# Optimization experiments

Measured on AMD Instinct MI355X. Metric: run time of the kernel, lower is better.

## Reference

```python
import jax, jax.numpy as jnp
import numpy as np

B, S, D, H = 1, 2048, 2048, 16
HD = D // H  # head_dim = 128
EPS = 1e-6


def setup_inputs() -> dict:
    key = jax.random.key(0)
    ks = jax.random.split(key, 12)
    sc = 0.02
    x = jax.random.normal(ks[0], (B, S, D), jnp.float32)
    wq = jax.random.normal(ks[1], (D, D), jnp.float32) * sc
    bq = jnp.zeros((D,), jnp.float32)
    wk = jax.random.normal(ks[2], (D, D), jnp.float32) * sc
    bk = jnp.zeros((D,), jnp.float32)
    wv = jax.random.normal(ks[3], (D, D), jnp.float32) * sc
    bv = jnp.zeros((D,), jnp.float32)
    wo = jax.random.normal(ks[4], (D, D), jnp.float32) * sc
    bo = jnp.zeros((D,), jnp.float32)
    gq = jnp.ones((D,), jnp.float32)  # RMSNorm weight for q
    gk = jnp.ones((D,), jnp.float32)  # RMSNorm weight for k
    # Rotary frequency table: complex freqs = cos + i*sin, shape [S, 1, HD//2]
    pos = jnp.arange(S, dtype=jnp.float32)
    inv = 1.0 / (10000.0 ** (jnp.arange(0, HD, 2, dtype=jnp.float32) / HD))  # [HD//2]
    theta = pos[:, None] * inv[None, :]  # [S, HD//2]
    freqs_cos = jnp.cos(theta)[:, None, :]  # [S, 1, HD//2]
    freqs_sin = jnp.sin(theta)[:, None, :]
    return {"x": x, "wq": wq, "bq": bq, "wk": wk, "bk": bk, "wv": wv, "bv": bv,
            "wo": wo, "bo": bo, "gq": gq, "gk": gk,
            "freqs_cos": freqs_cos, "freqs_sin": freqs_sin}


def _rmsnorm(x, g):
    # RMSNorm over full model dim (applied BEFORE head split, as in source)
    return x * jax.lax.rsqrt(jnp.mean(x * x, axis=-1, keepdims=True) + EPS) * g


def _rope(x, cos, sin):
    # x: [B,S,D] -> (B,S,H,HD//2,2) complex pairs; complex mult by (cos + i sin)
    b, s, d = x.shape
    xr = x.reshape(b, s, H, HD // 2, 2)
    a, bb = xr[..., 0], xr[..., 1]
    # cos/sin [S,1,HD//2] broadcast against [B,S,H,HD//2]
    ra = a * cos - bb * sin
    rb = a * sin + bb * cos
    return jnp.stack([ra, rb], axis=-1).reshape(b, s, d)


def reference(x, wq, bq, wk, bk, wv, bv, wo, bo, gq, gk, freqs_cos, freqs_sin):
    b, s, d = x.shape
    q = _rope(_rmsnorm(x @ wq.T + bq, gq), freqs_cos, freqs_sin)
    k = _rope(_rmsnorm(x @ wk.T + bk, gk), freqs_cos, freqs_sin)
    v = x @ wv.T + bv
    qh = q.reshape(b, s, H, HD).transpose(0, 2, 1, 3)  # [B,H,S,HD]
    kh = k.reshape(b, s, H, HD).transpose(0, 2, 1, 3)
    vh = v.reshape(b, s, H, HD).transpose(0, 2, 1, 3)
    scores = jnp.einsum('bhqd,bhkd->bhqk', qh, kh) / np.sqrt(HD).astype(np.float32)
    attn = jax.nn.softmax(scores, axis=-1)
    out = jnp.einsum('bhqk,bhkd->bhqd', attn, vh)
    out = out.transpose(0, 2, 1, 3).reshape(b, s, d)
    return out @ wo.T + bo
```

## Files before the change

kernel.cpp:

```cpp
#include <hip/hip_runtime.h>
#include <math.h>

typedef unsigned short u16;
typedef unsigned int u32;
typedef __bf16 bf16x8 __attribute__((ext_vector_type(8)));
typedef float f32x4 __attribute__((ext_vector_type(4)));
typedef float f32x16 __attribute__((ext_vector_type(16)));

__device__ __forceinline__ u16 f2bf(float f) {
  unsigned u = __float_as_uint(f);
  u += 0x7fff + ((u >> 16) & 1);
  return (u16)(u >> 16);
}

__device__ __forceinline__ u32 cvtpk(float lo, float hi) {
  u32 r;
  asm("v_cvt_pk_bf16_f32 %0, %1, %2" : "=v"(r) : "v"(lo), "v"(hi));
  return r;
}

__device__ __forceinline__ void pswap(u32& x, u32& y) {
  asm volatile("v_permlane32_swap_b32 %0, %1" : "+v"(x), "+v"(y));
}

__device__ __forceinline__ void gload_lds16(const void* g, void* l) {
  __builtin_amdgcn_global_load_lds(
      (const __attribute__((address_space(1))) unsigned int*)g,
      (__attribute__((address_space(3))) unsigned int*)l, 16, 0, 0);
}

__global__ __launch_bounds__(256) void k_cvt5(const float* __restrict__ s0,
                                              const float* __restrict__ s1,
                                              const float* __restrict__ s2,
                                              const float* __restrict__ s3,
                                              const float* __restrict__ s4,
                                              u16* __restrict__ dx,
                                              u16* __restrict__ dqkv,
                                              u16* __restrict__ dwo) {
  const int y = blockIdx.y;
  const float* s = (y == 0) ? s0 : (y == 1) ? s1 : (y == 2) ? s2
                   : (y == 3) ? s3 : s4;
  u16* d = (y == 0) ? dx : (y == 4) ? dwo : dqkv + (size_t)(y - 1) * 4194304;
  int i = (blockIdx.x * 256 + threadIdx.x) * 4;
  float4 v = *(const float4*)(s + i);
  ushort4 o;
  o.x = f2bf(v.x); o.y = f2bf(v.y); o.z = f2bf(v.z); o.w = f2bf(v.w);
  *(ushort4*)(d + i) = o;
}

__global__ __launch_bounds__(512, 4) void k_gemm_big(const u16* __restrict__ A,
                                                     const u16* __restrict__ B,
                                                     float* __restrict__ C,
                                                     int M, int N, int K) {
  __shared__ __align__(16) char lds[2][40960];
  const int tid = threadIdx.x;
  const int wid = tid >> 6, lane = tid & 63;
  const int lr = lane & 15, lg = lane >> 4;
  const int wm = (wid >> 2) * 64, wn = (wid & 3) * 48;
  const int nbx = N / 192, nby = M >> 7;
  const int colsPerXcd = nbx >> 3;
  const int xcd = blockIdx.x & 7, idx = blockIdx.x >> 3;
  const int bx = xcd * colsPerXcd + idx / nby;
  const int by = idx % nby;
  const int bm = by * 128, bn = bx * 192;
  const int srow = tid >> 3;
  const int schunk = (tid & 7) ^ (srow & 7);
  const size_t rsK = (size_t)K * 2;
  const char* gA = (const char*)A + (size_t)(bm + srow) * rsK + schunk * 16;
  const char* gB = (const char*)B + (size_t)(bn + srow) * rsK + schunk * 16;
  char* dA = (char*)lds + wid * 1024;
  char* dB = (char*)lds + 16384 + wid * 1024;

#define STAGE(cur, k0)                                                         \
  {                                                                            \
    _Pragma("unroll") for (int i = 0; i < 2; ++i)                              \
        gload_lds16(gA + (size_t)(i * 64) * rsK + (size_t)(k0) * 2,            \
                    dA + (cur) * 40960 + i * 8192);                            \
    _Pragma("unroll") for (int i = 0; i < 3; ++i)                              \
        gload_lds16(gB + (size_t)(i * 64) * rsK + (size_t)(k0) * 2,            \
                    dB + (cur) * 40960 + i * 8192);                            \
  }

  f32x4 acc[4][3] = {};
  STAGE(0, 0);
  STAGE(1, 64);
  asm volatile("s_waitcnt vmcnt(5)" ::: "memory");
  __builtin_amdgcn_s_barrier();
  const int NT = K >> 6;
  int cur = 0;
  const int rsw = (lr & 7);
  for (int t = 0; t < NT; ++t) {
    const char* La = (const char*)lds + cur * 40960;
    const char* Lb = La + 16384;
    bf16x8 af[4][2], bfr[3][2];
#pragma unroll
    for (int mi = 0; mi < 4; ++mi)
#pragma unroll
      for (int kk = 0; kk < 2; ++kk)
        af[mi][kk] = *(const bf16x8*)(La + (wm + mi * 16 + lr) * 128 +
                                      (((kk * 4 + lg) ^ rsw) * 16));
#pragma unroll
    for (int ni = 0; ni < 3; ++ni)
#pragma unroll
      for (int kk = 0; kk < 2; ++kk)
        bfr[ni][kk] = *(const bf16x8*)(Lb + (wn + ni * 16 + lr) * 128 +
                                       (((kk * 4 + lg) ^ rsw) * 16));
    asm volatile("s_waitcnt lgkmcnt(0)" ::: "memory");
    __builtin_amdgcn_s_barrier();
    if (t + 2 < NT) STAGE(cur, (t + 2) << 6);
    __builtin_amdgcn_s_setprio(1);
#pragma unroll
    for (int kk = 0; kk < 2; ++kk)
#pragma unroll
      for (int mi = 0; mi < 4; ++mi)
#pragma unroll
        for (int ni = 0; ni < 3; ++ni)
          acc[mi][ni] = __builtin_amdgcn_mfma_f32_16x16x32_bf16(
              af[mi][kk], bfr[ni][kk], acc[mi][ni], 0, 0, 0);
    __builtin_amdgcn_s_setprio(0);
    if (t + 2 < NT)
      asm volatile("s_waitcnt vmcnt(5)" ::: "memory");
    else
      asm volatile("s_waitcnt vmcnt(0)" ::: "memory");
    __builtin_amdgcn_s_barrier();
    cur ^= 1;
  }
#undef STAGE
#pragma unroll
  for (int mi = 0; mi < 4; ++mi)
#pragma unroll
    for (int ni = 0; ni < 3; ++ni)
#pragma unroll
      for (int j = 0; j < 4; ++j)
        C[(size_t)(bm + wm + mi * 16 + lg * 4 + j) * N + bn + wn + ni * 16 + lr] =
            acc[mi][ni][j];
}

__global__ __launch_bounds__(256, 2) void k_gemm_pipe(const u16* __restrict__ A,
                                                      const u16* __restrict__ B,
                                                      const float* __restrict__ bias,
                                                      float* __restrict__ C,
                                                      int M, int N, int K) {
  __shared__ __align__(16) char lds[2][24576];
  const int tid = threadIdx.x;
  const int wid = tid >> 6, lane = tid & 63;
  const int lr = lane & 15, lg = lane >> 4;
  const int wm = (wid >> 1) * 64, wn = (wid & 1) * 32;
  const int nbx = N >> 6, nby = M >> 7;
  const int colsPerXcd = nbx >> 3;
  const int xcd = blockIdx.x & 7, idx = blockIdx.x >> 3;
  const int bx = xcd * colsPerXcd + idx / nby;
  const int by = idx % nby;
  const int bm = by * 128, bn = bx * 64;
  const int srow = tid >> 3;
  const int schunk = (tid & 7) ^ (srow & 7);
  const size_t rsK = (size_t)K * 2;
  const char* gA = (const char*)A + (size_t)(bm + srow) * rsK + schunk * 16;
  const char* gB = (const char*)B + (size_t)(bn + srow) * rsK + schunk * 16;
  char* dA = (char*)lds + wid * 1024;
  char* dB = (char*)lds + 16384 + wid * 1024;

#define STAGE(cur, k0)                                                         \
  {                                                                            \
    _Pragma("unroll") for (int i = 0; i < 4; ++i)                              \
        gload_lds16(gA + (size_t)(i * 32) * rsK + (size_t)(k0) * 2,            \
                    dA + (cur) * 24576 + i * 4096);                            \
    _Pragma("unroll") for (int i = 0; i < 2; ++i)                              \
        gload_lds16(gB + (size_t)(i * 32) * rsK + (size_t)(k0) * 2,            \
                    dB + (cur) * 24576 + i * 4096);                            \
  }

  f32x4 acc[4][2] = {};
  STAGE(0, 0);
  STAGE(1, 64);
  asm volatile("s_waitcnt vmcnt(6)" ::: "memory");
  __builtin_amdgcn_s_barrier();
  const int NT = K >> 6;
  int cur = 0;
  const int rsw = (lr & 7);
  for (int t = 0; t < NT; ++t) {
    const char* La = (const char*)lds + cur * 24576;
    const char* Lb = La + 16384;
    bf16x8 af[4][2], bfr[2][2];
#pragma unroll
    for (int mi = 0; mi < 4; ++mi)
#pragma unroll
      for (int kk = 0; kk < 2; ++kk)
        af[mi][kk] = *(const bf16x8*)(La + (wm + mi * 16 + lr) * 128 +
                                      (((kk * 4 + lg) ^ rsw) * 16));
#pragma unroll
    for (int ni = 0; ni < 2; ++ni)
#pragma unroll
      for (int kk = 0; kk < 2; ++kk)
        bfr[ni][kk] = *(const bf16x8*)(Lb + (wn + ni * 16 + lr) * 128 +
                                       (((kk * 4 + lg) ^ rsw) * 16));
    asm volatile("s_waitcnt lgkmcnt(0)" ::: "memory");
    __builtin_amdgcn_s_barrier();
    if (t + 2 < NT) STAGE(cur, (t + 2) << 6);
    __builtin_amdgcn_s_setprio(1);
#pragma unroll
    for (int kk = 0; kk < 2; ++kk)
#pragma unroll
      for (int mi = 0; mi < 4; ++mi)
#pragma unroll
        for (int ni = 0; ni < 2; ++ni)
          acc[mi][ni] = __builtin_amdgcn_mfma_f32_16x16x32_bf16(
              af[mi][kk], bfr[ni][kk], acc[mi][ni], 0, 0, 0);
    __builtin_amdgcn_s_setprio(0);
    if (t + 2 < NT)
      asm volatile("s_waitcnt vmcnt(6)" ::: "memory");
    else
      asm volatile("s_waitcnt vmcnt(0)" ::: "memory");
    __builtin_amdgcn_s_barrier();
    cur ^= 1;
  }
#undef STAGE
#pragma unroll
  for (int mi = 0; mi < 4; ++mi)
#pragma unroll
    for (int ni = 0; ni < 2; ++ni) {
      int col = bn + wn + ni * 16 + lr;
      float bb = bias[col];
#pragma unroll
      for (int j = 0; j < 4; ++j)
        C[(size_t)(bm + wm + mi * 16 + lg * 4 + j) * N + col] =
            acc[mi][ni][j] + bb;
    }
}

__global__ __launch_bounds__(256) void k_rmsnorm_rope(
    const float* __restrict__ qkv, const float* __restrict__ bq,
    const float* __restrict__ bk, const float* __restrict__ gq,
    const float* __restrict__ gk, const float* __restrict__ fcos,
    const float* __restrict__ fsin, u16* __restrict__ qb, u16* __restrict__ kb) {
  const int s = blockIdx.x, which = blockIdx.y;
  const int t = threadIdx.x;
  const float* src = qkv + (size_t)s * 6144 + which * 2048;
  const float* bias = which ? bk : bq;
  const float* g = which ? gk : gq;
  u16* dst = (which ? kb : qb) + (size_t)s * 2048;
  const int c0 = t * 8;
  float4 a0 = *(const float4*)(src + c0);
  float4 a1 = *(const float4*)(src + c0 + 4);
  float4 b0 = *(const float4*)(bias + c0);
  float4 b1 = *(const float4*)(bias + c0 + 4);
  float v[8];
  v[0] = a0.x + b0.x; v[1] = a0.y + b0.y; v[2] = a0.z + b0.z; v[3] = a0.w + b0.w;
  v[4] = a1.x + b1.x; v[5] = a1.y + b1.y; v[6] = a1.z + b1.z; v[7] = a1.w + b1.w;
  float ss = 0.f;
#pragma unroll
  for (int j = 0; j < 8; ++j) ss += v[j] * v[j];
#pragma unroll
  for (int m = 1; m < 64; m <<= 1) ss += __shfl_xor(ss, m);
  __shared__ float red[4];
  if ((t & 63) == 0) red[t >> 6] = ss;
  __syncthreads();
  float r = rsqrtf((red[0] + red[1] + red[2] + red[3]) * (1.0f / 2048.0f) + 1e-6f);
  if (!which) r *= 0.08838834764831843f * 1.4426950408889634f;
  float4 g0 = *(const float4*)(g + c0);
  float4 g1 = *(const float4*)(g + c0 + 4);
  float gg[8] = {g0.x, g0.y, g0.z, g0.w, g1.x, g1.y, g1.z, g1.w};
  const int p0 = (c0 & 127) >> 1;
  u16 o[8];
#pragma unroll
  for (int j = 0; j < 4; ++j) {
    float a = v[2 * j] * r * gg[2 * j];
    float b = v[2 * j + 1] * r * gg[2 * j + 1];
    float co = fcos[s * 64 + p0 + j], si = fsin[s * 64 + p0 + j];
    o[2 * j]     = f2bf(a * co - b * si);
    o[2 * j + 1] = f2bf(a * si + b * co);
  }
  ushort4 q0; q0.x = o[0]; q0.y = o[1]; q0.z = o[2]; q0.w = o[3];
  ushort4 q1; q1.x = o[4]; q1.y = o[5]; q1.z = o[6]; q1.w = o[7];
  *(ushort4*)(dst + c0) = q0;
  *(ushort4*)(dst + c0 + 4) = q1;
}

__global__ __launch_bounds__(256) void k_transpose_v(const float* __restrict__ qkv,
                                                     const float* __restrict__ bv,
                                                     u16* __restrict__ vT) {
  __shared__ float tile[64][65];
  const int s0 = blockIdx.x * 64, d0 = blockIdx.y * 64;
  const int t = threadIdx.x;
  const int tc = (t & 15) * 4, tr = t >> 4;
  float4 bb = *(const float4*)(bv + d0 + tc);
#pragma unroll
  for (int i = 0; i < 4; ++i) {
    int sr = tr + i * 16;
    float4 x = *(const float4*)(qkv + (size_t)(s0 + sr) * 6144 + 4096 + d0 + tc);
    tile[sr][tc + 0] = x.x + bb.x;
    tile[sr][tc + 1] = x.y + bb.y;
    tile[sr][tc + 2] = x.z + bb.z;
    tile[sr][tc + 3] = x.w + bb.w;
  }
  __syncthreads();
#pragma unroll
  for (int i = 0; i < 4; ++i) {
    int dr = tr + i * 16;
    ushort4 o;
    o.x = f2bf(tile[tc + 0][dr]);
    o.y = f2bf(tile[tc + 1][dr]);
    o.z = f2bf(tile[tc + 2][dr]);
    o.w = f2bf(tile[tc + 3][dr]);
    *(ushort4*)(vT + (size_t)(d0 + dr) * 2048 + s0 + tc) = o;
  }
}

__global__ __launch_bounds__(256, 3) void k_attn(const u16* __restrict__ qb,
                                                 const u16* __restrict__ kb,
                                                 const u16* __restrict__ vT,
                                                 float* __restrict__ opart,
                                                 float* __restrict__ ml) {
  __shared__ __align__(16) char Ks[2][16384];
  __shared__ __align__(16) char Vs[16384];
  const int bid = blockIdx.x;
  const int xcd = bid & 7, j = bid >> 3;
  const int h = xcd * 2 + (j & 1);
  const int qt = (j >> 1) & 15;
  const int ks = j >> 5;
  const int tid = threadIdx.x;
  const int wid = tid >> 6, lane = tid & 63;
  const int l31 = lane & 31, hi = lane >> 5;
  const int q0w = qt * 128 + wid * 32;
  const char* kbB = (const char*)kb;
  const char* vTB = (const char*)vT;
  const int krow = tid >> 4;
  const int kc = (tid & 15) ^ krow;
  const int vrow = tid >> 3;
  const int vc = (tid & 7) ^ (vrow & 7);

#define STAGE_K(buf, k0)                                                       \
  {                                                                            \
    _Pragma("unroll") for (int i = 0; i < 4; ++i)                              \
        gload_lds16(kbB + (size_t)((k0) + i * 16 + krow) * 4096 + h * 256 +    \
                        kc * 16,                                               \
                    (char*)Ks + (buf) * 16384 + i * 4096 + wid * 1024);        \
  }
#define STAGE_V(k0)                                                            \
  {                                                                            \
    _Pragma("unroll") for (int i = 0; i < 4; ++i)                              \
        gload_lds16(vTB + (size_t)(h * 128 + i * 32 + vrow) * 4096 +           \
                        (size_t)(k0) * 2 + vc * 16,                            \
                    (char*)Vs + i * 4096 + wid * 1024);                        \
  }

  bf16x8 qf[8];
#pragma unroll
  for (int ds = 0; ds < 8; ++ds)
    qf[ds] = *(const bf16x8*)(qb + (size_t)(q0w + l31) * 2048 + h * 128 +
                              ds * 16 + hi * 8);
  f32x16 o[4] = {};
  float mrun = -3.0e38f, lsum = 0.f;
  const int kbeg = ks * 1024;
  const int ksw = l31 & 15, vsw = l31 & 7;
  STAGE_K(0, kbeg);
  int cur = 0;
  for (int t = 0; t < 16; ++t) {
    __builtin_amdgcn_s_barrier();
    STAGE_V(kbeg + t * 64);
    if (t < 15) {
      STAGE_K(cur ^ 1, kbeg + (t + 1) * 64);
      asm volatile("s_waitcnt vmcnt(8)" ::: "memory");
    } else {
      asm volatile("s_waitcnt vmcnt(4)" ::: "memory");
    }
    __builtin_amdgcn_s_barrier();
    const char* Kc = Ks[cur];
    f32x16 p0 = {}, p1 = {};
    __builtin_amdgcn_s_setprio(1);
#pragma unroll
    for (int ds = 0; ds < 8; ++ds) {
      bf16x8 kf0 = *(const bf16x8*)(Kc + l31 * 256 + (((ds * 2 + hi) ^ ksw) * 16));
      p0 = __builtin_amdgcn_mfma_f32_32x32x16_bf16(kf0, qf[ds], p0, 0, 0, 0);
      bf16x8 kf1 = *(const bf16x8*)(Kc + (32 + l31) * 256 +
                                    (((ds * 2 + hi) ^ ksw) * 16));
      p1 = __builtin_amdgcn_mfma_f32_32x32x16_bf16(kf1, qf[ds], p1, 0, 0, 0);
    }
    __builtin_amdgcn_s_setprio(0);
    {
      float tm[8];
#pragma unroll
      for (int r = 0; r < 8; ++r)
        tm[r] = fmaxf(fmaxf(p0[2 * r], p0[2 * r + 1]),
                      fmaxf(p1[2 * r], p1[2 * r + 1]));
#pragma unroll
      for (int s = 4; s > 0; s >>= 1)
#pragma unroll
        for (int r = 0; r < s; ++r) tm[r] = fmaxf(tm[r], tm[r + s]);
      float pm = fmaxf(tm[0], __shfl_xor(tm[0], 32));
      if (!__all(pm <= mrun + 8.0f)) {
        float nm = fmaxf(mrun, pm);
        float fv = __builtin_amdgcn_exp2f(mrun - nm);
#pragma unroll
        for (int dt = 0; dt < 4; ++dt) o[dt] *= fv;
        lsum *= fv;
        mrun = nm;
      }
    }
    {
#pragma unroll
      for (int r = 0; r < 16; ++r) p0[r] = __builtin_amdgcn_exp2f(p0[r] - mrun);
#pragma unroll
      for (int r = 0; r < 16; ++r) p1[r] = __builtin_amdgcn_exp2f(p1[r] - mrun);
      float ts[8];
#pragma unroll
      for (int r = 0; r < 8; ++r)
        ts[r] = (p0[2 * r] + p0[2 * r + 1]) + (p1[2 * r] + p1[2 * r + 1]);
#pragma unroll
      for (int s = 4; s > 0; s >>= 1)
#pragma unroll
        for (int r = 0; r < s; ++r) ts[r] += ts[r + s];
      lsum += ts[0] + __shfl_xor(ts[0], 32);
    }
    bf16x8 pa[4];
#pragma unroll
    for (int sl = 0; sl < 2; ++sl) {
      u32 E0 = cvtpk(p0[8 * sl + 0], p0[8 * sl + 1]);
      u32 E1 = cvtpk(p0[8 * sl + 2], p0[8 * sl + 3]);
      u32 O0 = cvtpk(p0[8 * sl + 4], p0[8 * sl + 5]);
      u32 O1 = cvtpk(p0[8 * sl + 6], p0[8 * sl + 7]);
      pswap(E0, O0); pswap(E1, O1);
      union { u32 w[4]; bf16x8 v; } uu;
      uu.w[0] = E0; uu.w[1] = E1; uu.w[2] = O0; uu.w[3] = O1;
      pa[sl] = uu.v;
    }
#pragma unroll
    for (int sl = 0; sl < 2; ++sl) {
      u32 E0 = cvtpk(p1[8 * sl + 0], p1[8 * sl + 1]);
      u32 E1 = cvtpk(p1[8 * sl + 2], p1[8 * sl + 3]);
      u32 O0 = cvtpk(p1[8 * sl + 4], p1[8 * sl + 5]);
      u32 O1 = cvtpk(p1[8 * sl + 6], p1[8 * sl + 7]);
      pswap(E0, O0); pswap(E1, O1);
      union { u32 w[4]; bf16x8 v; } uu;
      uu.w[0] = E0; uu.w[1] = E1; uu.w[2] = O0; uu.w[3] = O1;
      pa[2 + sl] = uu.v;
    }
    if (t < 15)
      asm volatile("s_waitcnt vmcnt(4)" ::: "memory");
    else
      asm volatile("s_waitcnt vmcnt(0)" ::: "memory");
    __builtin_amdgcn_s_barrier();
    __builtin_amdgcn_s_setprio(1);
#pragma unroll
    for (int s = 0; s < 4; ++s)
#pragma unroll
      for (int dt = 0; dt < 4; ++dt) {
        bf16x8 vf = *(const bf16x8*)((const char*)Vs + (dt * 32 + l31) * 128 +
                                     (((s * 2 + hi) ^ vsw) * 16));
        o[dt] = __builtin_amdgcn_mfma_f32_32x32x16_bf16(pa[s], vf, o[dt], 0, 0, 0);
      }
    __builtin_amdgcn_s_setprio(0);
    cur ^= 1;
  }
#undef STAGE_K
#undef STAGE_V
  float* opb = opart + ((size_t)ks * 32768 + (size_t)h * 2048 + q0w) * 128 + l31;
#pragma unroll
  for (int dt = 0; dt < 4; ++dt)
#pragma unroll
    for (int r = 0; r < 16; ++r)
      opb[(size_t)((r & 3) + 8 * (r >> 2) + 4 * hi) * 128 + dt * 32] = o[dt][r];
  if (lane < 32) {
    float2 v2; v2.x = mrun; v2.y = lsum;
    *(float2*)(ml + ((size_t)ks * 32768 + (size_t)h * 2048 + q0w + l31) * 2) = v2;
  }
}

__global__ __launch_bounds__(256) void k_attn_merge(const float* __restrict__ opart,
                                                    const float* __restrict__ ml,
                                                    u16* __restrict__ ob) {
  const int r = blockIdx.x * 8 + (threadIdx.x >> 5);
  const int d0 = (threadIdx.x & 31) * 4;
  float2 ml0 = *(const float2*)(ml + (size_t)r * 2);
  float2 ml1 = *(const float2*)(ml + (size_t)(32768 + r) * 2);
  float M = fmaxf(ml0.x, ml1.x);
  float f0 = __builtin_amdgcn_exp2f(ml0.x - M);
  float f1 = __builtin_amdgcn_exp2f(ml1.x - M);
  float inv = 1.0f / (ml0.y * f0 + ml1.y * f1);
  float4 a = *(const float4*)(opart + (size_t)r * 128 + d0);
  float4 b = *(const float4*)(opart + (size_t)(32768 + r) * 128 + d0);
  int h = r >> 11, q = r & 2047;
  ushort4 o;
  o.x = f2bf((a.x * f0 + b.x * f1) * inv);
  o.y = f2bf((a.y * f0 + b.y * f1) * inv);
  o.z = f2bf((a.z * f0 + b.z * f1) * inv);
  o.w = f2bf((a.w * f0 + b.w * f1) * inv);
  *(ushort4*)(ob + (size_t)q * 2048 + h * 128 + d0) = o;
}

extern "C" void kernel_launch(void* const* d_in, const int* in_sizes, int n_in,
                              void* d_out, int out_size, void* d_ws, size_t ws_size,
                              hipStream_t stream) {
  const float* x    = (const float*)d_in[0];
  const float* wq   = (const float*)d_in[1];
  const float* bq   = (const float*)d_in[2];
  const float* wk   = (const float*)d_in[3];
  const float* bk   = (const float*)d_in[4];
  const float* wv   = (const float*)d_in[5];
  const float* bv   = (const float*)d_in[6];
  const float* wo   = (const float*)d_in[7];
  const float* bo   = (const float*)d_in[8];
  const float* gq   = (const float*)d_in[9];
  const float* gk   = (const float*)d_in[10];
  const float* fcos = (const float*)d_in[11];
  const float* fsin = (const float*)d_in[12];

  char* ws = (char*)d_ws;
  float* qkv_pre = (float*)ws;
  float* opart = (float*)ws;
  float* ml    = (float*)(ws + 33554432);
  u16* xb   = (u16*)(ws + 50331648);
  u16* wqkv = (u16*)(ws + 58720256);
  u16* qb   = (u16*)(ws + 50331648);
  u16* kb   = (u16*)(ws + 58720256);
  u16* vT   = (u16*)(ws + 67108864);
  u16* ao   = (u16*)(ws + 75497472);
  u16* wob  = (u16*)(ws + 83886080);

  k_cvt5<<<dim3(4096, 5), 256, 0, stream>>>(x, wq, wk, wv, wo, xb, wqkv, wob);

  k_gemm_big<<<512, 512, 0, stream>>>(xb, wqkv, qkv_pre, 2048, 6144, 2048);
  k_rmsnorm_rope<<<dim3(2048, 2), 256, 0, stream>>>(qkv_pre, bq, bk, gq, gk,
                                                    fcos, fsin, qb, kb);
  k_transpose_v<<<dim3(32, 32), 256, 0, stream>>>(qkv_pre, bv, vT);
  k_attn<<<512, 256, 0, stream>>>(qb, kb, vT, opart, ml);
  k_attn_merge<<<4096, 256, 0, stream>>>(opart, ml, ao);
  k_gemm_pipe<<<dim3(512), 256, 0, stream>>>(ao, wob, bo, (float*)d_out,
                                             2048, 2048, 2048);
}
```

Measured before the change: 170.5 us.

## Double-buffer both K and V tiles in attention with one barrier per step

```diff
diff --git a/kernel.cpp b/kernel.cpp
--- a/kernel.cpp
+++ b/kernel.cpp
@@ -306,13 +306,13 @@
   }
 }
 
-__global__ __launch_bounds__(256, 3) void k_attn(const u16* __restrict__ qb,
+__global__ __launch_bounds__(256, 2) void k_attn(const u16* __restrict__ qb,
                                                  const u16* __restrict__ kb,
                                                  const u16* __restrict__ vT,
                                                  float* __restrict__ opart,
                                                  float* __restrict__ ml) {
   __shared__ __align__(16) char Ks[2][16384];
-  __shared__ __align__(16) char Vs[16384];
+  __shared__ __align__(16) char Vs[2][16384];
   const int bid = blockIdx.x;
   const int xcd = bid & 7, j = bid >> 3;
   const int h = xcd * 2 + (j & 1);
@@ -329,19 +329,16 @@
   const int vrow = tid >> 3;
   const int vc = (tid & 7) ^ (vrow & 7);
 
-#define STAGE_K(buf, k0)                                                       \
+#define STAGE(buf, k0)                                                         \
   {                                                                            \
     _Pragma("unroll") for (int i = 0; i < 4; ++i)                              \
         gload_lds16(kbB + (size_t)((k0) + i * 16 + krow) * 4096 + h * 256 +    \
                         kc * 16,                                               \
                     (char*)Ks + (buf) * 16384 + i * 4096 + wid * 1024);        \
-  }
-#define STAGE_V(k0)                                                            \
-  {                                                                            \
     _Pragma("unroll") for (int i = 0; i < 4; ++i)                              \
         gload_lds16(vTB + (size_t)(h * 128 + i * 32 + vrow) * 4096 +           \
                         (size_t)(k0) * 2 + vc * 16,                            \
-                    (char*)Vs + i * 4096 + wid * 1024);                        \
+                    (char*)Vs + (buf) * 16384 + i * 4096 + wid * 1024);        \
   }
 
   bf16x8 qf[8];
@@ -353,19 +350,13 @@
   float mrun = -3.0e38f, lsum = 0.f;
   const int kbeg = ks * 1024;
   const int ksw = l31 & 15, vsw = l31 & 7;
-  STAGE_K(0, kbeg);
+  STAGE(0, kbeg);
+  __syncthreads();
   int cur = 0;
   for (int t = 0; t < 16; ++t) {
-    __builtin_amdgcn_s_barrier();
-    STAGE_V(kbeg + t * 64);
-    if (t < 15) {
-      STAGE_K(cur ^ 1, kbeg + (t + 1) * 64);
-      asm volatile("s_waitcnt vmcnt(8)" ::: "memory");
-    } else {
-      asm volatile("s_waitcnt vmcnt(4)" ::: "memory");
-    }
-    __builtin_amdgcn_s_barrier();
+    if (t + 1 < 16) STAGE(cur ^ 1, kbeg + (t + 1) * 64);
     const char* Kc = Ks[cur];
+    const char* Vc = Vs[cur];
     f32x16 p0 = {}, p1 = {};
     __builtin_amdgcn_s_setprio(1);
 #pragma unroll
@@ -435,25 +426,20 @@
       uu.w[0] = E0; uu.w[1] = E1; uu.w[2] = O0; uu.w[3] = O1;
       pa[2 + sl] = uu.v;
     }
-    if (t < 15)
-      asm volatile("s_waitcnt vmcnt(4)" ::: "memory");
-    else
-      asm volatile("s_waitcnt vmcnt(0)" ::: "memory");
-    __builtin_amdgcn_s_barrier();
     __builtin_amdgcn_s_setprio(1);
 #pragma unroll
     for (int s = 0; s < 4; ++s)
 #pragma unroll
       for (int dt = 0; dt < 4; ++dt) {
-        bf16x8 vf = *(const bf16x8*)((const char*)Vs + (dt * 32 + l31) * 128 +
+        bf16x8 vf = *(const bf16x8*)(Vc + (dt * 32 + l31) * 128 +
                                      (((s * 2 + hi) ^ vsw) * 16));
         o[dt] = __builtin_amdgcn_mfma_f32_32x32x16_bf16(pa[s], vf, o[dt], 0, 0, 0);
       }
     __builtin_amdgcn_s_setprio(0);
+    __syncthreads();
     cur ^= 1;
   }
-#undef STAGE_K
-#undef STAGE_V
+#undef STAGE
   float* opb = opart + ((size_t)ks * 32768 + (size_t)h * 2048 + q0w) * 128 + l31;
 #pragma unroll
   for (int dt = 0; dt < 4; ++dt)
```

Measured after the change: 159.1 us. 6.7% less time.
